# Kernel optimization log

Hardware: AMD Instinct MI355X
Metric: run time of the kernel (lower is better)

Reference implementation:

```python
import jax, jax.numpy as jnp
import numpy as np

B, C_IN, C_OUT, F, K = 4, 64, 64, 50000, 16
BN_EPS = 1e-5


def setup_inputs() -> dict:
    key = jax.random.key(0)
    k1, k2, k3, k4 = jax.random.split(key, 4)
    fea = jax.random.normal(k1, (B, C_IN, F), dtype=jnp.float32)
    ring_n = jax.random.randint(k2, (B, F, K), 0, F, dtype=jnp.int64)
    # Conv1d(kernel_size=1) weight [out, in] and bias [out]
    W = jax.random.normal(k3, (C_OUT, C_IN), dtype=jnp.float32) / np.sqrt(C_IN)
    b = jax.random.normal(k4, (C_OUT,), dtype=jnp.float32) * 0.01
    gamma = jnp.ones((C_OUT,), dtype=jnp.float32)
    beta = jnp.zeros((C_OUT,), dtype=jnp.float32)
    return {"fea": fea, "ring_n": ring_n, "W": W, "b": b, "gamma": gamma, "beta": beta}


def reference(fea, ring_n, W, b, gamma, beta):
    # Note: original torch code overwrites the cat result, so only the
    # NEIGHBOR features are summed (center face excluded).
    def gather_sum(f, r):  # f: [C, F], r: [F, K]
        return f[:, r].sum(axis=-1)  # [C, F, K] -> [C, F]

    summed = jax.vmap(gather_sum)(fea, ring_n)  # [B, C_in, F]
    # 1x1 conv == channel matmul
    y = jnp.einsum("oc,bcf->bof", W, summed) + b[None, :, None]  # [B, C_out, F]
    # BatchNorm1d (training mode): stats over (batch, faces) per channel
    mean = y.mean(axis=(0, 2), keepdims=True)
    var = y.var(axis=(0, 2), keepdims=True)  # biased, as torch BN uses for normalization
    y = (y - mean) * jax.lax.rsqrt(var + BN_EPS)
    y = y * gamma[None, :, None] + beta[None, :, None]
    return jax.nn.relu(y)
```

## Files before the change

### kernel.cpp

```cpp
#include <hip/hip_runtime.h>
#include <hip/hip_bf16.h>
#include <stdint.h>

#define Bn 4
#define Cn 64
#define Fn 50000
#define Kn 16
#define NTOT (Bn*Fn)
#define EPS 1e-5f
#define ROWB 136

typedef unsigned short u16;
typedef unsigned int u32;
typedef __attribute__((ext_vector_type(8))) short short8;
typedef __attribute__((ext_vector_type(4))) float f32x4;

__device__ __forceinline__ u16 f2bf(float x) {
  __hip_bfloat16 h = __float2bfloat16(x);
  return *reinterpret_cast<u16*>(&h);
}
__device__ __forceinline__ u32 pack2(float a, float b) {
  return (u32)f2bf(a) | ((u32)f2bf(b) << 16);
}

__global__ __launch_bounds__(256) void k1_mfma(
    const float* __restrict__ fea, const float* __restrict__ W,
    u32* __restrict__ Gt) {
  const int b = blockIdx.y;
  const int f0 = blockIdx.x * 256;
  const int t = threadIdx.x;
  const int l = t & 63;
  const int quad = l >> 4;
  __shared__ char a_s[256 * ROWB];

  short8 afr[4][2];
  #pragma unroll
  for (int ot = 0; ot < 4; ot++) {
    #pragma unroll
    for (int kk = 0; kk < 2; kk++) {
      const float* wr = W + (ot * 16 + (l & 15)) * 64 + kk * 32 + quad * 8;
      float4 wa = *(const float4*)wr;
      float4 wb = *(const float4*)(wr + 4);
      union { short8 v; u32 u[4]; } fr;
      fr.u[0] = pack2(wa.x, wa.y); fr.u[1] = pack2(wa.z, wa.w);
      fr.u[2] = pack2(wb.x, wb.y); fr.u[3] = pack2(wb.z, wb.w);
      afr[ot][kk] = fr.v;
    }
  }

  {
    const float* fb_ = fea + ((size_t)b * Cn) * Fn;
    #pragma unroll
    for (int i = 0; i < 32; i++) {
      int cp = (t >> 6) + 4 * (i >> 2);
      int fl = (t & 63) + 64 * (i & 3);
      int fg = f0 + fl;
      float va = 0.f, vb = 0.f;
      if (fg < Fn) {
        va = fb_[(size_t)(2 * cp) * Fn + fg];
        vb = fb_[(size_t)(2 * cp + 1) * Fn + fg];
      }
      *(u32*)(a_s + fl * ROWB + 4 * cp) = pack2(va, vb);
    }
  }
  __syncthreads();

  const int wv = t >> 6;
  f32x4 acc[4][4];
  #pragma unroll
  for (int ot = 0; ot < 4; ot++)
    #pragma unroll
    for (int ft = 0; ft < 4; ft++) acc[ot][ft] = (f32x4){0.f, 0.f, 0.f, 0.f};

  #pragma unroll
  for (int ft = 0; ft < 4; ft++) {
    int frow = wv * 64 + ft * 16 + (l & 15);
    char* p = a_s + frow * ROWB + quad * 16;
    union { short8 v; uint2 u[2]; } b0, b1;
    b0.u[0] = *(uint2*)(p);      b0.u[1] = *(uint2*)(p + 8);
    b1.u[0] = *(uint2*)(p + 64); b1.u[1] = *(uint2*)(p + 72);
    #pragma unroll
    for (int ot = 0; ot < 4; ot++) {
      acc[ot][ft] = __builtin_amdgcn_mfma_f32_16x16x32_bf16(afr[ot][0], b0.v, acc[ot][ft], 0, 0, 0);
      acc[ot][ft] = __builtin_amdgcn_mfma_f32_16x16x32_bf16(afr[ot][1], b1.v, acc[ot][ft], 0, 0, 0);
    }
  }

  #pragma unroll
  for (int ot = 0; ot < 4; ot++) {
    #pragma unroll
    for (int ft = 0; ft < 4; ft++) {
      int fg = f0 + wv * 64 + ft * 16 + (l & 15);
      if (fg < Fn) {
        uint2 pv;
        pv.x = pack2(acc[ot][ft][0], acc[ot][ft][1]);
        pv.y = pack2(acc[ot][ft][2], acc[ot][ft][3]);
        *(uint2*)(Gt + ((size_t)(b * 4 + ot) * Fn + fg) * 8 + quad * 2) = pv;
      }
    }
  }
}

template<int WRITE_BF16>
__global__ __launch_bounds__(256) void k2_gather(
    const u32* __restrict__ Gt, const int* __restrict__ ring,
    const float* __restrict__ bias, u32* __restrict__ Y, float* __restrict__ outF,
    float* __restrict__ gsum, float* __restrict__ gsum2) {
  const int bid = blockIdx.x;
  const int combo = bid & 15;
  const int ft = bid >> 4;
  const int b = combo >> 2;
  const int seg = combo & 3;
  const int t = threadIdx.x;
  const int face_l = t >> 1;
  const int half = t & 1;
  const int fa = ft * 128 + face_l;
  const bool valid = fa < Fn;

  __shared__ float y_s[128][17];
  __shared__ float rs[16][17];
  __shared__ float rs2[16][17];

  float acc[8];
  #pragma unroll
  for (int i = 0; i < 8; i++) acc[i] = 0.f;

  const int c0 = seg * 16 + half * 8;
  float bv[8];
  #pragma unroll
  for (int i = 0; i < 8; i++) bv[i] = bias[c0 + i];

  if (valid) {
    const int4* rp = (const int4*)(ring + ((size_t)b * Fn + fa) * Kn);
    int4 i0 = rp[0], i1 = rp[1], i2 = rp[2], i3 = rp[3];
    int idx[16] = {i0.x,i0.y,i0.z,i0.w, i1.x,i1.y,i1.z,i1.w,
                   i2.x,i2.y,i2.z,i2.w, i3.x,i3.y,i3.z,i3.w};
    const uint4* Gs = (const uint4*)(Gt + (size_t)combo * Fn * 8);
    uint4 v[16];
    #pragma unroll
    for (int k = 0; k < 16; k++) v[k] = Gs[(size_t)idx[k] * 2 + half];
    #pragma unroll
    for (int k = 0; k < 16; k++) {
      u32 uu[4] = {v[k].x, v[k].y, v[k].z, v[k].w};
      #pragma unroll
      for (int p = 0; p < 4; p++) {
        acc[2*p]   += __uint_as_float(uu[p] << 16);
        acc[2*p+1] += __uint_as_float(uu[p] & 0xffff0000u);
      }
    }
  }
  #pragma unroll
  for (int i = 0; i < 8; i++) acc[i] = valid ? acc[i] + bv[i] : 0.f;
  #pragma unroll
  for (int i = 0; i < 8; i++) y_s[face_l][half * 8 + i] = acc[i];
  __syncthreads();

  if (WRITE_BF16) {
    const int fp = t & 63, chb = t >> 6;
    const int fa2 = ft * 64 + fp;
    if (fa2 * 2 < Fn) {
      #pragma unroll
      for (int j = 0; j < 4; j++) {
        int ch = chb * 4 + j;
        Y[((size_t)b * 64 + seg * 16 + ch) * (Fn / 2) + fa2] =
            pack2(y_s[fp * 2][ch], y_s[fp * 2 + 1][ch]);
      }
    }
  } else {
    const int fl2 = t & 127, chb = t >> 7;
    if (ft * 128 + fl2 < Fn) {
      float* ob = outF + ((size_t)b * 64 + seg * 16 + chb * 8) * Fn + ft * 128 + fl2;
      #pragma unroll
      for (int j = 0; j < 8; j++) ob[(size_t)j * Fn] = y_s[fl2][chb * 8 + j];
    }
  }

  {
    const int ch = t & 15, part = t >> 4;
    float s = 0.f, s2 = 0.f;
    #pragma unroll
    for (int i = 0; i < 8; i++) {
      float v = y_s[part * 8 + i][ch];
      s += v; s2 += v * v;
    }
    rs[part][ch] = s; rs2[part][ch] = s2;
  }
  __syncthreads();
  if (t < 16) {
    float s = 0.f;
    #pragma unroll
    for (int p = 0; p < 16; p++) s += rs[p][t];
    atomicAdd(&gsum[seg * 16 + t], s);
  } else if (t < 32) {
    const int ch = t - 16;
    float s2 = 0.f;
    #pragma unroll
    for (int p = 0; p < 16; p++) s2 += rs2[p][ch];
    atomicAdd(&gsum2[seg * 16 + ch], s2);
  }
}

__global__ void k3_stats(const float* __restrict__ gsum, const float* __restrict__ gsum2,
                         const float* __restrict__ gamma, const float* __restrict__ beta,
                         float* __restrict__ ab) {
  int o = threadIdx.x;
  if (o < 64) {
    float inv = 1.0f / (float)NTOT;
    float mean = gsum[o] * inv;
    float var = gsum2[o] * inv - mean * mean;
    float r = rsqrtf(var + EPS);
    float a = gamma[o] * r;
    ab[o] = a;
    ab[64 + o] = beta[o] - mean * a;
  }
}

__global__ __launch_bounds__(256) void k4_norm_bf(const u32* __restrict__ Y,
                                                  const float* __restrict__ ab,
                                                  float* __restrict__ out) {
  const int combo = blockIdx.x & 15;
  const int chunk = blockIdx.x >> 4;
  const int b = combo >> 2;
  const int seg = combo & 3;
  const int pos = chunk * 256 + threadIdx.x;
  if (pos >= 12500) return;
  #pragma unroll
  for (int j = 0; j < 16; j++) {
    int ch = seg * 16 + j;
    float a = ab[ch], cc = ab[64 + ch];
    uint2 u = ((const uint2*)Y)[((size_t)b * 64 + ch) * 12500 + pos];
    float4 v;
    v.x = __uint_as_float(u.x << 16);
    v.y = __uint_as_float(u.x & 0xffff0000u);
    v.z = __uint_as_float(u.y << 16);
    v.w = __uint_as_float(u.y & 0xffff0000u);
    v.x = fmaxf(fmaf(v.x, a, cc), 0.f);
    v.y = fmaxf(fmaf(v.y, a, cc), 0.f);
    v.z = fmaxf(fmaf(v.z, a, cc), 0.f);
    v.w = fmaxf(fmaf(v.w, a, cc), 0.f);
    ((float4*)out)[((size_t)b * 64 + ch) * 12500 + pos] = v;
  }
}

__global__ __launch_bounds__(256) void k4_norm_f32(float* __restrict__ out,
                                                   const float* __restrict__ ab) {
  int i = blockIdx.x * 256 + threadIdx.x;
  int o = (i / (Fn / 4)) & 63;
  float a = ab[o], c = ab[64 + o];
  float4 v = ((float4*)out)[i];
  v.x = fmaxf(fmaf(v.x, a, c), 0.f);
  v.y = fmaxf(fmaf(v.y, a, c), 0.f);
  v.z = fmaxf(fmaf(v.z, a, c), 0.f);
  v.w = fmaxf(fmaf(v.w, a, c), 0.f);
  ((float4*)out)[i] = v;
}

extern "C" void kernel_launch(void* const* d_in, const int* in_sizes, int n_in,
                              void* d_out, int out_size, void* d_ws, size_t ws_size,
                              hipStream_t stream) {
  const float* fea   = (const float*)d_in[0];
  const int*   ring  = (const int*)d_in[1];
  const float* W     = (const float*)d_in[2];
  const float* bias  = (const float*)d_in[3];
  const float* gamma = (const float*)d_in[4];
  const float* beta  = (const float*)d_in[5];
  float* out = (float*)d_out;

  u32* Gt = (u32*)d_ws;
  const size_t gtBytes = (size_t)Bn * 4 * Fn * 8 * 4;
  const size_t yBytes  = (size_t)Bn * 64 * (Fn / 2) * 4;
  const bool bf16y = ws_size >= gtBytes + yBytes + 1024;

  u32* Y = (u32*)((char*)d_ws + gtBytes);
  float* gsum  = bf16y ? (float*)((char*)d_ws + gtBytes + yBytes)
                       : (float*)((char*)d_ws + gtBytes);
  float* gsum2 = gsum + 64;
  float* ab    = gsum + 128;

  hipMemsetAsync(gsum, 0, 2 * 64 * sizeof(float), stream);
  k1_mfma<<<dim3((Fn + 255) / 256, Bn), 256, 0, stream>>>(fea, W, Gt);
  const int ftiles = (Fn + 127) / 128;
  if (bf16y) {
    k2_gather<1><<<dim3(ftiles * 16), 256, 0, stream>>>(Gt, ring, bias, Y, out, gsum, gsum2);
    k3_stats<<<1, 64, 0, stream>>>(gsum, gsum2, gamma, beta, ab);
    const int chunks = (12500 + 255) / 256;
    k4_norm_bf<<<dim3(chunks * 16), 256, 0, stream>>>(Y, ab, out);
  } else {
    k2_gather<0><<<dim3(ftiles * 16), 256, 0, stream>>>(Gt, ring, bias, Y, out, gsum, gsum2);
    k3_stats<<<1, 64, 0, stream>>>(gsum, gsum2, gamma, beta, ab);
    k4_norm_f32<<<dim3((Bn * Cn * Fn / 4) / 256), 256, 0, stream>>>(out, ab);
  }
}
```

Before: 215.2 us.

## Load fea directly into MFMA fragments, split gather loads, fold BN stats into norm

The first kernel drops its LDS staging and syncthreads. Each lane now reads its 16 channel values straight from global memory into bf16 MFMA fragments. The gather kernel issues its 16 neighbour loads as two batches of 8, which may lower register pressure. The separate stats kernel is removed: the normalize kernel recomputes mean, variance and the scale/shift per thread and processes 8 bf16 values per thread with 128-bit loads. The trade is strided, less coalesced global reads in the MFMA kernel and redundant per-thread stat arithmetic, in exchange for one fewer launch and no LDS round trip.

```diff
diff --git a/kernel.cpp b/kernel.cpp
--- a/kernel.cpp
+++ b/kernel.cpp
@@ -8,7 +8,6 @@
 #define Kn 16
 #define NTOT (Bn*Fn)
 #define EPS 1e-5f
-#define ROWB 136
 
 typedef unsigned short u16;
 typedef unsigned int u32;
@@ -31,14 +30,15 @@
   const int t = threadIdx.x;
   const int l = t & 63;
   const int quad = l >> 4;
-  __shared__ char a_s[256 * ROWB];
+  const int lane15 = l & 15;
+  const int wv = t >> 6;
 
   short8 afr[4][2];
   #pragma unroll
   for (int ot = 0; ot < 4; ot++) {
     #pragma unroll
     for (int kk = 0; kk < 2; kk++) {
-      const float* wr = W + (ot * 16 + (l & 15)) * 64 + kk * 32 + quad * 8;
+      const float* wr = W + (ot * 16 + lane15) * 64 + kk * 32 + quad * 8;
       float4 wa = *(const float4*)wr;
       float4 wb = *(const float4*)(wr + 4);
       union { short8 v; u32 u[4]; } fr;
@@ -48,24 +48,7 @@
     }
   }
 
-  {
-    const float* fb_ = fea + ((size_t)b * Cn) * Fn;
-    #pragma unroll
-    for (int i = 0; i < 32; i++) {
-      int cp = (t >> 6) + 4 * (i >> 2);
-      int fl = (t & 63) + 64 * (i & 3);
-      int fg = f0 + fl;
-      float va = 0.f, vb = 0.f;
-      if (fg < Fn) {
-        va = fb_[(size_t)(2 * cp) * Fn + fg];
-        vb = fb_[(size_t)(2 * cp + 1) * Fn + fg];
-      }
-      *(u32*)(a_s + fl * ROWB + 4 * cp) = pack2(va, vb);
-    }
-  }
-  __syncthreads();
-
-  const int wv = t >> 6;
+  const float* fb = fea + (size_t)b * Cn * Fn;
   f32x4 acc[4][4];
   #pragma unroll
   for (int ot = 0; ot < 4; ot++)
@@ -74,15 +57,25 @@
 
   #pragma unroll
   for (int ft = 0; ft < 4; ft++) {
-    int frow = wv * 64 + ft * 16 + (l & 15);
-    char* p = a_s + frow * ROWB + quad * 16;
-    union { short8 v; uint2 u[2]; } b0, b1;
-    b0.u[0] = *(uint2*)(p);      b0.u[1] = *(uint2*)(p + 8);
-    b1.u[0] = *(uint2*)(p + 64); b1.u[1] = *(uint2*)(p + 72);
+    const int fg = f0 + wv * 64 + ft * 16 + lane15;
+    const bool v = fg < Fn;
+    float x[16];
+    #pragma unroll
+    for (int j = 0; j < 8; j++)
+      x[j] = v ? fb[(size_t)(quad * 8 + j) * Fn + fg] : 0.f;
+    #pragma unroll
+    for (int j = 0; j < 8; j++)
+      x[8 + j] = v ? fb[(size_t)(32 + quad * 8 + j) * Fn + fg] : 0.f;
+    union { short8 s; u32 u[4]; } b0, b1;
+    #pragma unroll
+    for (int p = 0; p < 4; p++) {
+      b0.u[p] = pack2(x[2 * p], x[2 * p + 1]);
+      b1.u[p] = pack2(x[8 + 2 * p], x[8 + 2 * p + 1]);
+    }
     #pragma unroll
     for (int ot = 0; ot < 4; ot++) {
-      acc[ot][ft] = __builtin_amdgcn_mfma_f32_16x16x32_bf16(afr[ot][0], b0.v, acc[ot][ft], 0, 0, 0);
-      acc[ot][ft] = __builtin_amdgcn_mfma_f32_16x16x32_bf16(afr[ot][1], b1.v, acc[ot][ft], 0, 0, 0);
+      acc[ot][ft] = __builtin_amdgcn_mfma_f32_16x16x32_bf16(afr[ot][0], b0.s, acc[ot][ft], 0, 0, 0);
+      acc[ot][ft] = __builtin_amdgcn_mfma_f32_16x16x32_bf16(afr[ot][1], b1.s, acc[ot][ft], 0, 0, 0);
     }
   }
 
@@ -90,7 +83,7 @@
   for (int ot = 0; ot < 4; ot++) {
     #pragma unroll
     for (int ft = 0; ft < 4; ft++) {
-      int fg = f0 + wv * 64 + ft * 16 + (l & 15);
+      int fg = f0 + wv * 64 + ft * 16 + lane15;
       if (fg < Fn) {
         uint2 pv;
         pv.x = pack2(acc[ot][ft][0], acc[ot][ft][1]);
@@ -136,12 +129,23 @@
     int idx[16] = {i0.x,i0.y,i0.z,i0.w, i1.x,i1.y,i1.z,i1.w,
                    i2.x,i2.y,i2.z,i2.w, i3.x,i3.y,i3.z,i3.w};
     const uint4* Gs = (const uint4*)(Gt + (size_t)combo * Fn * 8);
-    uint4 v[16];
-    #pragma unroll
-    for (int k = 0; k < 16; k++) v[k] = Gs[(size_t)idx[k] * 2 + half];
-    #pragma unroll
-    for (int k = 0; k < 16; k++) {
+    uint4 v[8], w[8];
+    #pragma unroll
+    for (int k = 0; k < 8; k++) v[k] = Gs[(size_t)idx[k] * 2 + half];
+    #pragma unroll
+    for (int k = 0; k < 8; k++) w[k] = Gs[(size_t)idx[8 + k] * 2 + half];
+    #pragma unroll
+    for (int k = 0; k < 8; k++) {
       u32 uu[4] = {v[k].x, v[k].y, v[k].z, v[k].w};
+      #pragma unroll
+      for (int p = 0; p < 4; p++) {
+        acc[2*p]   += __uint_as_float(uu[p] << 16);
+        acc[2*p+1] += __uint_as_float(uu[p] & 0xffff0000u);
+      }
+    }
+    #pragma unroll
+    for (int k = 0; k < 8; k++) {
+      u32 uu[4] = {w[k].x, w[k].y, w[k].z, w[k].w};
       #pragma unroll
       for (int p = 0; p < 4; p++) {
         acc[2*p]   += __uint_as_float(uu[p] << 16);
@@ -215,31 +219,29 @@
   }
 }
 
-__global__ __launch_bounds__(256) void k4_norm_bf(const u32* __restrict__ Y,
-                                                  const float* __restrict__ ab,
-                                                  float* __restrict__ out) {
-  const int combo = blockIdx.x & 15;
-  const int chunk = blockIdx.x >> 4;
-  const int b = combo >> 2;
-  const int seg = combo & 3;
-  const int pos = chunk * 256 + threadIdx.x;
-  if (pos >= 12500) return;
-  #pragma unroll
-  for (int j = 0; j < 16; j++) {
-    int ch = seg * 16 + j;
-    float a = ab[ch], cc = ab[64 + ch];
-    uint2 u = ((const uint2*)Y)[((size_t)b * 64 + ch) * 12500 + pos];
-    float4 v;
-    v.x = __uint_as_float(u.x << 16);
-    v.y = __uint_as_float(u.x & 0xffff0000u);
-    v.z = __uint_as_float(u.y << 16);
-    v.w = __uint_as_float(u.y & 0xffff0000u);
-    v.x = fmaxf(fmaf(v.x, a, cc), 0.f);
-    v.y = fmaxf(fmaf(v.y, a, cc), 0.f);
-    v.z = fmaxf(fmaf(v.z, a, cc), 0.f);
-    v.w = fmaxf(fmaf(v.w, a, cc), 0.f);
-    ((float4*)out)[((size_t)b * 64 + ch) * 12500 + pos] = v;
-  }
+__global__ __launch_bounds__(256) void k4_norm_bf(
+    const u32* __restrict__ Y, const float* __restrict__ gsum,
+    const float* __restrict__ gsum2, const float* __restrict__ gamma,
+    const float* __restrict__ beta, float* __restrict__ out) {
+  int i = blockIdx.x * 256 + threadIdx.x;
+  int ch = (i / 6250) & 63;
+  const float inv = 1.0f / (float)NTOT;
+  float mean = gsum[ch] * inv;
+  float var = gsum2[ch] * inv - mean * mean;
+  float a = gamma[ch] * rsqrtf(var + EPS);
+  float cc = beta[ch] - mean * a;
+  uint4 u = ((const uint4*)Y)[i];
+  u32 uu[4] = {u.x, u.y, u.z, u.w};
+  float r[8];
+  #pragma unroll
+  for (int p = 0; p < 4; p++) {
+    r[2*p]   = fmaxf(fmaf(__uint_as_float(uu[p] << 16), a, cc), 0.f);
+    r[2*p+1] = fmaxf(fmaf(__uint_as_float(uu[p] & 0xffff0000u), a, cc), 0.f);
+  }
+  float4 o0 = make_float4(r[0], r[1], r[2], r[3]);
+  float4 o1 = make_float4(r[4], r[5], r[6], r[7]);
+  ((float4*)out)[i * 2] = o0;
+  ((float4*)out)[i * 2 + 1] = o1;
 }
 
 __global__ __launch_bounds__(256) void k4_norm_f32(float* __restrict__ out,
@@ -282,9 +284,7 @@
   const int ftiles = (Fn + 127) / 128;
   if (bf16y) {
     k2_gather<1><<<dim3(ftiles * 16), 256, 0, stream>>>(Gt, ring, bias, Y, out, gsum, gsum2);
-    k3_stats<<<1, 64, 0, stream>>>(gsum, gsum2, gamma, beta, ab);
-    const int chunks = (12500 + 255) / 256;
-    k4_norm_bf<<<dim3(chunks * 16), 256, 0, stream>>>(Y, ab, out);
+    k4_norm_bf<<<dim3(Bn * 64 * 6250 / 256), 256, 0, stream>>>(Y, gsum, gsum2, gamma, beta, out);
   } else {
     k2_gather<0><<<dim3(ftiles * 16), 256, 0, stream>>>(Gt, ring, bias, Y, out, gsum, gsum2);
     k3_stats<<<1, 64, 0, stream>>>(gsum, gsum2, gamma, beta, ab);
```

Result: slower. 236.1 us (+9.7%).
